# Performance work log

Measured on AMD Instinct MI355X. Metric: run time of the kernel, lower is better.

Reference implementation:

```python
import jax, jax.numpy as jnp
import numpy as np

MEMORY_LENGTH = 32   # past states remembered
N_TARGETS = 3        # leak sources
T_STEPS = 1000       # duration / dt
DT = 0.1
HIDDEN = 128         # policy MLP hidden width
N_AGENTS = 1024      # vmapped batch of rollouts
IN_DIM = MEMORY_LENGTH * 3 + MEMORY_LENGTH  # flattened x_hist + conc_hist


def setup_inputs() -> dict:
    key = jax.random.key(0)
    k0, k1, k2, k3, k4 = jax.random.split(key, 5)
    target_pos = jax.random.normal(k0, (N_TARGETS, 2), dtype=jnp.float32) * 5.0
    logsigma = jax.random.normal(k1, (N_TARGETS,), dtype=jnp.float32) * 0.5
    x_inits = jax.random.normal(k2, (N_AGENTS, 3), dtype=jnp.float32) * 2.0
    W1 = jax.random.normal(k3, (HIDDEN, IN_DIM), dtype=jnp.float32) / np.sqrt(IN_DIM).astype(np.float32)
    b1 = jnp.zeros((HIDDEN,), dtype=jnp.float32)
    W2 = jax.random.normal(k4, (2, HIDDEN), dtype=jnp.float32) / np.sqrt(HIDDEN).astype(np.float32)
    b2 = jnp.zeros((2,), dtype=jnp.float32)
    return {"target_pos": target_pos, "logsigma": logsigma, "x_inits": x_inits,
            "W1": W1, "b1": b1, "W2": W2, "b2": b2}


def _concentration(x, y, target_pos, sigma):
    # x, y: [N]; target_pos: [nt, 2]; sigma: [nt] -> conc: [N]
    d2 = (x[:, None] - target_pos[None, :, 0]) ** 2 + (y[:, None] - target_pos[None, :, 1]) ** 2
    return ((1.0 / sigma) * jnp.exp(-d2 / sigma)).sum(-1)


def reference(target_pos, logsigma, x_inits, W1, b1, W2, b2):
    sigma = jnp.exp(logsigma)
    N = x_inits.shape[0]
    # initial histories: memory_length copies of the initial state / concentration
    x_hist0 = jnp.tile(x_inits[:, None, :], (1, MEMORY_LENGTH, 1))        # [N, M, 3]
    conc0 = _concentration(x_inits[:, 0], x_inits[:, 1], target_pos, sigma)
    conc_hist0 = jnp.tile(conc0[:, None], (1, MEMORY_LENGTH))             # [N, M]

    def step(carry, _):
        x_hist, conc_hist, x_cur = carry
        # policy MLP on flattened histories -> tanh controls (v, omega)
        feats = jnp.concatenate([x_hist.reshape(N, -1), conc_hist], axis=-1)  # [N, 4M]
        h = jax.nn.relu(feats @ W1.T + b1)
        u = jnp.tanh(h @ W2.T + b2)                                            # [N, 2]
        v, w = u[:, 0], u[:, 1]
        th = x_cur[:, 2]
        # Dubins car dynamics (zero actuation noise)
        x_next = x_cur + DT * jnp.stack([v * jnp.cos(th), v * jnp.sin(th), w], axis=-1)
        # shift histories: drop oldest, insert newest at front
        x_hist = jnp.concatenate([x_next[:, None, :], x_hist[:, :-1, :]], axis=1)
        c = _concentration(x_next[:, 0], x_next[:, 1], target_pos, sigma)
        conc_hist = jnp.concatenate([c[:, None], conc_hist[:, :-1]], axis=1)
        return (x_hist, conc_hist, x_next), (x_next, u)

    _, (traj, ctrl) = jax.lax.scan(step, (x_hist0, conc_hist0, x_inits), None, length=T_STEPS)
    # traj: [T, N, 3], ctrl: [T, N, 2]
    d2 = ((traj[:, :, 0][..., None] - target_pos[None, None, :, 0]) ** 2
          + (traj[:, :, 1][..., None] - target_pos[None, None, :, 1]) ** 2)   # [T, N, nt]
    per_target = (-1.0 / sigma) * jnp.exp(-d2 / sigma)                        # [T, N, nt]
    cost = per_target.mean(axis=(0, 1)).sum() + (ctrl ** 2).mean()
    return cost
```

## Files before the change

### kernel.cpp

```cpp
#include <hip/hip_runtime.h>

#define T_STEPS 1000
#define DT 0.1f
#define HIDDEN 128
#define N_AGENTS 1024

typedef float v2f __attribute__((ext_vector_type(2)));

__device__ __forceinline__ float tanh_fast(float x) {
    float e = __expf(2.0f * x);
    return 1.0f - 2.0f * __builtin_amdgcn_rcpf(e + 1.0f);
}

__device__ __forceinline__ v2f opaque_load8(const float* p) {
    v2f v;
    asm volatile("global_load_dwordx2 %0, %1, off\n\ts_waitcnt vmcnt(0)"
                 : "=v"(v)
                 : "v"((unsigned long long)(uintptr_t)p)
                 : "memory");
    return v;
}

__device__ __forceinline__ float uniformf(float v) {
    return __builtin_bit_cast(float,
        __builtin_amdgcn_readfirstlane(__builtin_bit_cast(int, v)));
}

__device__ __forceinline__ float wave_sum_dpp(float x) {
    float t;
    #define DPPADD(ctrl, rmask)                                              \
        t = __builtin_bit_cast(float, __builtin_amdgcn_update_dpp(           \
                0, __builtin_bit_cast(int, x), ctrl, rmask, 0xf, false));    \
        x += t;
    DPPADD(0x111, 0xf)
    DPPADD(0x112, 0xf)
    DPPADD(0x114, 0xf)
    DPPADD(0x118, 0xf)
    DPPADD(0x142, 0xa)
    DPPADD(0x143, 0xc)
    #undef DPPADD
    return __builtin_bit_cast(float,
        __builtin_amdgcn_readlane(__builtin_bit_cast(int, x), 63));
}

__global__ void pack_kernel(const float* __restrict__ W1,
                            float* __restrict__ pw) {
    const int row = blockIdx.x;
    const int a   = threadIdx.x;
    const float* rp = W1 + row * 128;
    float* out = pw + row * 128;
    out[2*a]          = rp[3*a];
    out[2*a + 1]      = rp[3*a + 1];
    out[64 + 2*a]     = rp[3*a + 2];
    out[64 + 2*a + 1] = rp[96 + a];
}

__global__ __launch_bounds__(128)
__attribute__((amdgpu_waves_per_eu(2, 2)))
void sim_kernel(const float* __restrict__ target_pos,
                const float* __restrict__ logsigma,
                const float* __restrict__ x_inits,
                const float* __restrict__ pw,
                const float* __restrict__ b1,
                const float* __restrict__ W2,
                const float* __restrict__ b2,
                float2* __restrict__ ws) {
    const int agent = blockIdx.x;
    const int tid  = threadIdx.x;
    const int h    = tid >> 6;
    const int lane = tid & 63;
    const int rowA = lane;
    const int rowB = lane + 64;

    __shared__ float2 part1[32][64];
    __shared__ float4 e4buf[16];

    const float tx0 = uniformf(target_pos[0]), ty0 = uniformf(target_pos[1]);
    const float tx1 = uniformf(target_pos[2]), ty1 = uniformf(target_pos[3]);
    const float tx2 = uniformf(target_pos[4]), ty2 = uniformf(target_pos[5]);
    const float is0 = uniformf(1.0f / expf(logsigma[0]));
    const float is1 = uniformf(1.0f / expf(logsigma[1]));
    const float is2 = uniformf(1.0f / expf(logsigma[2]));

    v2f WxyA[16], WzcA[16], WxyB[16], WzcB[16];
    {
        const float* baseA = pw + rowA * 128;
        const float* baseB = pw + rowB * 128;
        #pragma unroll
        for (int i = 0; i < 16; ++i) {
            WxyA[i] = opaque_load8(baseA + 32 * h + 2 * i);
            WzcA[i] = opaque_load8(baseA + 64 + 32 * h + 2 * i);
            WxyB[i] = opaque_load8(baseB + 32 * h + 2 * i);
            WzcB[i] = opaque_load8(baseB + 64 + 32 * h + 2 * i);
        }
    }
    const float b1A = b1[rowA], b1B = b1[rowB];
    const float w20A = W2[rowA], w20B = W2[rowB];
    const float w21A = W2[HIDDEN + rowA], w21B = W2[HIDDEN + rowB];
    const float b2x = uniformf(b2[0]), b2y = uniformf(b2[1]);

    auto conc = [&](float px, float py) {
        float dx0 = px - tx0, dy0 = py - ty0;
        float dx1 = px - tx1, dy1 = py - ty1;
        float dx2 = px - tx2, dy2 = py - ty2;
        float cc  = is0 * __expf(-(dx0*dx0 + dy0*dy0) * is0);
        cc       += is1 * __expf(-(dx1*dx1 + dy1*dy1) * is1);
        cc       += is2 * __expf(-(dx2*dx2 + dy2*dy2) * is2);
        return cc;
    };

    float x  = uniformf(x_inits[3 * agent]);
    float y  = uniformf(x_inits[3 * agent + 1]);
    float th = uniformf(x_inits[3 * agent + 2]);
    float c  = conc(x, y);

    v2f RA[16], RB[16];
    {
        v2f exy0 = {x, y}, ezc0 = {th, c};
        if (h == 0) {
            v2f aA = {0.f,0.f}, aB = {0.f,0.f};
            #pragma unroll
            for (int k = 15; k >= 0; --k) {
                aA = WxyA[k]*exy0 + aA;  aA = WzcA[k]*ezc0 + aA;
                aB = WxyB[k]*exy0 + aB;  aB = WzcB[k]*ezc0 + aB;
                RA[k] = aA;  RB[k] = aB;
            }
            if (lane == 0) {
                float4 e0 = make_float4(x, y, th, c);
                #pragma unroll
                for (int m = 9; m < 16; ++m) e4buf[m] = e0;
                e4buf[0] = e0;
            }
        } else {
            RA[8] = (v2f){0.f,0.f};  RB[8] = (v2f){0.f,0.f};
            v2f aA = {0.f,0.f}, aB = {0.f,0.f};
            #pragma unroll
            for (int k = 15; k >= 1; --k) {
                aA = WxyA[k]*exy0 + aA;  aA = WzcA[k]*ezc0 + aA;
                aB = WxyB[k]*exy0 + aB;  aB = WzcB[k]*ezc0 + aB;
                RA[(k+8)&15] = aA;  RB[(k+8)&15] = aB;
            }
            v2f fA = WxyA[0]*exy0 + aA;  fA = WzcA[0]*ezc0 + fA;
            v2f fB = WxyB[0]*exy0 + aB;  fB = WzcB[0]*ezc0 + fB;
            float2 full = make_float2(fA.x + fA.y, fB.x + fB.y);
            #pragma unroll
            for (int s = 0; s <= 8; ++s) part1[s][lane] = full;
        }
    }
    __syncthreads();

    float S_c = 0.f, S_u = 0.f;

    if (h == 0) {
        float2 pl = part1[0][lane];
        auto h0_step = [&](int j, int s16) {
            float hA = fmaxf((RA[j].x + RA[j].y) + pl.x + b1A, 0.f);
            float hB = fmaxf((RB[j].x + RB[j].y) + pl.y + b1B, 0.f);
            float s0 = wave_sum_dpp(fmaf(w20A, hA, w20B * hB));
            float s1 = wave_sum_dpp(fmaf(w21A, hA, w21B * hB));
            float v  = tanh_fast(s0 + b2x);
            float wv = tanh_fast(s1 + b2y);
            S_u += v * v + wv * wv;
            float sn = __sinf(th), cs = __cosf(th);
            float dv = DT * v;
            x  = fmaf(dv, cs, x);
            y  = fmaf(dv, sn, y);
            th = fmaf(DT, wv, th);
            c  = conc(x, y);
            S_c += c;
            if (lane == 0) e4buf[(j + 1) & 15] = make_float4(x, y, th, c);
            v2f exy = {x, y}, ezc = {th, c};
            RA[j] = WxyA[15] * exy;  RA[j] = WzcA[15] * ezc + RA[j];
            RB[j] = WxyB[15] * exy;  RB[j] = WzcB[15] * ezc + RB[j];
            #pragma unroll
            for (int k = 0; k < 15; ++k) {
                const int m = (j + 1 + k) & 15;
                RA[m] = WxyA[k] * exy + RA[m];  RA[m] = WzcA[k] * ezc + RA[m];
                RB[m] = WxyB[k] * exy + RB[m];  RB[m] = WzcB[k] * ezc + RB[m];
            }
            pl = part1[(s16 + j + 1) & 31][lane];
        };
        #pragma unroll 1
        for (int tt = 0; tt < 62; ++tt) {
            const int s16 = (tt & 1) << 4;
            __syncthreads();
            #pragma unroll
            for (int j = 0; j < 8; ++j) h0_step(j, s16);
            __syncthreads();
            #pragma unroll
            for (int j = 8; j < 16; ++j) h0_step(j, s16);
        }
        __syncthreads();
        #pragma unroll
        for (int j = 0; j < 8; ++j) h0_step(j, 0);

        if (lane == 0) ws[agent] = make_float2(S_c, S_u);
    } else {
        auto h1_step = [&](int j, int s16) {
            float4 e = e4buf[(j + 9) & 15];
            v2f exy = {e.x, e.y}, ezc = {e.z, e.w};
            {
                const int m = (j + 8) & 15;
                RA[m] = WxyA[15] * exy;  RA[m] = WzcA[15] * ezc + RA[m];
                RB[m] = WxyB[15] * exy;  RB[m] = WzcB[15] * ezc + RB[m];
            }
            #pragma unroll
            for (int k = 0; k < 15; ++k) {
                const int m = (j + 9 + k) & 15;
                RA[m] = WxyA[k] * exy + RA[m];  RA[m] = WzcA[k] * ezc + RA[m];
                RB[m] = WxyB[k] * exy + RB[m];  RB[m] = WzcB[k] * ezc + RB[m];
            }
            {
                const int m = (j + 9) & 15;
                part1[(s16 + j + 9) & 31][lane] =
                    make_float2(RA[m].x + RA[m].y, RB[m].x + RB[m].y);
            }
        };
        #pragma unroll 1
        for (int tt = 0; tt < 62; ++tt) {
            const int s16 = (tt & 1) << 4;
            __syncthreads();
            #pragma unroll
            for (int j = 0; j < 8; ++j) h1_step(j, s16);
            __syncthreads();
            #pragma unroll
            for (int j = 8; j < 16; ++j) h1_step(j, s16);
        }
        __syncthreads();
        #pragma unroll
        for (int j = 0; j < 8; ++j) h1_step(j, 0);
    }
}

__global__ void reduce_kernel(const float2* __restrict__ ws,
                              float* __restrict__ out) {
    const int tid = threadIdx.x;
    float sc = 0.f, su = 0.f;
    for (int i = tid; i < N_AGENTS; i += 256) {
        float2 v = ws[i];
        sc += v.x;
        su += v.y;
    }
    #pragma unroll
    for (int off = 32; off > 0; off >>= 1) {
        sc += __shfl_xor(sc, off);
        su += __shfl_xor(su, off);
    }
    __shared__ float2 partw[4];
    int wave = tid >> 6;
    if ((tid & 63) == 0) partw[wave] = make_float2(sc, su);
    __syncthreads();
    if (tid == 0) {
        float SC = partw[0].x + partw[1].x + partw[2].x + partw[3].x;
        float SU = partw[0].y + partw[1].y + partw[2].y + partw[3].y;
        const float invNT  = 1.0f / (float)(N_AGENTS * T_STEPS);
        const float invNT2 = 1.0f / (float)(N_AGENTS * T_STEPS * 2);
        out[0] = -SC * invNT + SU * invNT2;
    }
}

extern "C" void kernel_launch(void* const* d_in, const int* in_sizes, int n_in,
                              void* d_out, int out_size, void* d_ws, size_t ws_size,
                              hipStream_t stream) {
    const float* target_pos = (const float*)d_in[0];
    const float* logsigma   = (const float*)d_in[1];
    const float* x_inits    = (const float*)d_in[2];
    const float* W1         = (const float*)d_in[3];
    const float* b1         = (const float*)d_in[4];
    const float* W2         = (const float*)d_in[5];
    const float* b2         = (const float*)d_in[6];

    float*  pw   = (float*)d_ws;
    float2* sums = (float2*)((char*)d_ws + 64 * 1024);

    pack_kernel<<<HIDDEN, 32, 0, stream>>>(W1, pw);
    sim_kernel<<<N_AGENTS, 128, 0, stream>>>(target_pos, logsigma, x_inits,
                                             pw, b1, W2, b2, sums);
    reduce_kernel<<<1, 256, 0, stream>>>(sums, (float*)d_out);
}
```

Baseline: 655.3 us.

## Batch history-weight accumulation four steps at a time off the serial critical path

The wave that runs the sequential step loop now applies only the few weight updates needed for the next steps immediately. It defers the rest of the 16-deep history accumulation into a batched update after every four steps, which shortens the per-step latency chain. The helper wave likewise processes four history entries per batch using a sliding 20-entry accumulator, then writes partial sums and shifts. This cuts per-step dependency latency and lets the FMAs interleave better, at the cost of higher register pressure and more intricate index bookkeeping.

```diff
diff --git a/kernel.cpp b/kernel.cpp
--- a/kernel.cpp
+++ b/kernel.cpp
@@ -114,10 +114,10 @@
     float th = uniformf(x_inits[3 * agent + 2]);
     float c  = conc(x, y);
 
-    v2f RA[16], RB[16];
-    {
-        v2f exy0 = {x, y}, ezc0 = {th, c};
-        if (h == 0) {
+    if (h == 0) {
+        v2f RA[16], RB[16];
+        {
+            v2f exy0 = {x, y}, ezc0 = {th, c};
             v2f aA = {0.f,0.f}, aB = {0.f,0.f};
             #pragma unroll
             for (int k = 15; k >= 0; --k) {
@@ -131,31 +131,17 @@
                 for (int m = 9; m < 16; ++m) e4buf[m] = e0;
                 e4buf[0] = e0;
             }
-        } else {
-            RA[8] = (v2f){0.f,0.f};  RB[8] = (v2f){0.f,0.f};
-            v2f aA = {0.f,0.f}, aB = {0.f,0.f};
-            #pragma unroll
-            for (int k = 15; k >= 1; --k) {
-                aA = WxyA[k]*exy0 + aA;  aA = WzcA[k]*ezc0 + aA;
-                aB = WxyB[k]*exy0 + aB;  aB = WzcB[k]*ezc0 + aB;
-                RA[(k+8)&15] = aA;  RB[(k+8)&15] = aB;
-            }
-            v2f fA = WxyA[0]*exy0 + aA;  fA = WzcA[0]*ezc0 + fA;
-            v2f fB = WxyB[0]*exy0 + aB;  fB = WzcB[0]*ezc0 + fB;
-            float2 full = make_float2(fA.x + fA.y, fB.x + fB.y);
-            #pragma unroll
-            for (int s = 0; s <= 8; ++s) part1[s][lane] = full;
-        }
-    }
-    __syncthreads();
-
-    float S_c = 0.f, S_u = 0.f;
-
-    if (h == 0) {
+        }
+        __syncthreads();
         float2 pl = part1[0][lane];
+        v2f es_xy[4], es_zc[4];
+        float S_c = 0.f, S_u = 0.f;
+
         auto h0_step = [&](int j, int s16) {
             float hA = fmaxf((RA[j].x + RA[j].y) + pl.x + b1A, 0.f);
             float hB = fmaxf((RB[j].x + RB[j].y) + pl.y + b1B, 0.f);
+            RA[j] = (v2f){0.f, 0.f};
+            RB[j] = (v2f){0.f, 0.f};
             float s0 = wave_sum_dpp(fmaf(w20A, hA, w20B * hB));
             float s1 = wave_sum_dpp(fmaf(w21A, hA, w21B * hB));
             float v  = tanh_fast(s0 + b2x);
@@ -170,65 +156,121 @@
             S_c += c;
             if (lane == 0) e4buf[(j + 1) & 15] = make_float4(x, y, th, c);
             v2f exy = {x, y}, ezc = {th, c};
-            RA[j] = WxyA[15] * exy;  RA[j] = WzcA[15] * ezc + RA[j];
-            RB[j] = WxyB[15] * exy;  RB[j] = WzcB[15] * ezc + RB[j];
-            #pragma unroll
-            for (int k = 0; k < 15; ++k) {
-                const int m = (j + 1 + k) & 15;
-                RA[m] = WxyA[k] * exy + RA[m];  RA[m] = WzcA[k] * ezc + RA[m];
-                RB[m] = WxyB[k] * exy + RB[m];  RB[m] = WzcB[k] * ezc + RB[m];
+            es_xy[j & 3] = exy;  es_zc[j & 3] = ezc;
+            #pragma unroll
+            for (int k = 0; k < 3; ++k) {
+                if (k <= 2 - (j & 3)) {
+                    const int m = (j + 1 + k) & 15;
+                    RA[m] = WxyA[k]*exy + RA[m];  RA[m] = WzcA[k]*ezc + RA[m];
+                    RB[m] = WxyB[k]*exy + RB[m];  RB[m] = WzcB[k]*ezc + RB[m];
+                }
             }
             pl = part1[(s16 + j + 1) & 31][lane];
         };
+        auto h0_batch = [&](int q) {
+            #pragma unroll
+            for (int kk = 0; kk < 16; ++kk) {
+                #pragma unroll
+                for (int i = 0; i < 4; ++i) {
+                    if (kk >= 3 - i) {
+                        const int m = (4*q + i + 1 + kk) & 15;
+                        RA[m] = WxyA[kk]*es_xy[i] + RA[m];
+                        RA[m] = WzcA[kk]*es_zc[i] + RA[m];
+                        RB[m] = WxyB[kk]*es_xy[i] + RB[m];
+                        RB[m] = WzcB[kk]*es_zc[i] + RB[m];
+                    }
+                }
+            }
+        };
+
         #pragma unroll 1
-        for (int tt = 0; tt < 62; ++tt) {
-            const int s16 = (tt & 1) << 4;
+        for (int b = 0; b < 62; ++b) {
+            const int s16 = (b & 1) << 4;
             __syncthreads();
             #pragma unroll
-            for (int j = 0; j < 8; ++j) h0_step(j, s16);
+            for (int j = 0; j < 4; ++j) h0_step(j, s16);
+            h0_batch(0);
+            #pragma unroll
+            for (int j = 4; j < 8; ++j) h0_step(j, s16);
+            h0_batch(1);
             __syncthreads();
             #pragma unroll
-            for (int j = 8; j < 16; ++j) h0_step(j, s16);
+            for (int j = 8; j < 12; ++j) h0_step(j, s16);
+            h0_batch(2);
+            #pragma unroll
+            for (int j = 12; j < 16; ++j) h0_step(j, s16);
+            h0_batch(3);
         }
         __syncthreads();
         #pragma unroll
-        for (int j = 0; j < 8; ++j) h0_step(j, 0);
+        for (int j = 0; j < 4; ++j) h0_step(j, 0);
+        h0_batch(0);
+        #pragma unroll
+        for (int j = 4; j < 8; ++j) h0_step(j, 0);
 
         if (lane == 0) ws[agent] = make_float2(S_c, S_u);
     } else {
-        auto h1_step = [&](int j, int s16) {
-            float4 e = e4buf[(j + 9) & 15];
-            v2f exy = {e.x, e.y}, ezc = {e.z, e.w};
-            {
-                const int m = (j + 8) & 15;
-                RA[m] = WxyA[15] * exy;  RA[m] = WzcA[15] * ezc + RA[m];
-                RB[m] = WxyB[15] * exy;  RB[m] = WzcB[15] * ezc + RB[m];
-            }
-            #pragma unroll
-            for (int k = 0; k < 15; ++k) {
-                const int m = (j + 9 + k) & 15;
-                RA[m] = WxyA[k] * exy + RA[m];  RA[m] = WzcA[k] * ezc + RA[m];
-                RB[m] = WxyB[k] * exy + RB[m];  RB[m] = WzcB[k] * ezc + RB[m];
-            }
-            {
-                const int m = (j + 9) & 15;
-                part1[(s16 + j + 9) & 31][lane] =
-                    make_float2(RA[m].x + RA[m].y, RB[m].x + RB[m].y);
-            }
+        v2f PA[20], PB[20];
+        {
+            v2f exy0 = {x, y}, ezc0 = {th, c};
+            #pragma unroll
+            for (int i = 15; i < 20; ++i) { PA[i] = (v2f){0.f,0.f}; PB[i] = (v2f){0.f,0.f}; }
+            v2f aA = {0.f,0.f}, aB = {0.f,0.f};
+            #pragma unroll
+            for (int k = 15; k >= 1; --k) {
+                aA = WxyA[k]*exy0 + aA;  aA = WzcA[k]*ezc0 + aA;
+                aB = WxyB[k]*exy0 + aB;  aB = WzcB[k]*ezc0 + aB;
+                PA[k-1] = aA;  PB[k-1] = aB;
+            }
+            v2f fA = WxyA[0]*exy0 + aA;  fA = WzcA[0]*ezc0 + fA;
+            v2f fB = WxyB[0]*exy0 + aB;  fB = WzcB[0]*ezc0 + fB;
+            float2 full = make_float2(fA.x + fA.y, fB.x + fB.y);
+            #pragma unroll
+            for (int s = 0; s <= 8; ++s) part1[s][lane] = full;
+        }
+        __syncthreads();
+
+        auto h1_batch = [&](int n, int b1w) {
+            v2f pxy[4], pzc[4];
+            #pragma unroll
+            for (int i = 0; i < 4; ++i) {
+                float4 e = e4buf[(9 + 4*n + i) & 15];
+                pxy[i] = (v2f){e.x, e.y};
+                pzc[i] = (v2f){e.z, e.w};
+            }
+            #pragma unroll
+            for (int kk = 0; kk < 16; ++kk) {
+                #pragma unroll
+                for (int i = 0; i < 4; ++i) {
+                    const int idx = i + kk;
+                    PA[idx] = WxyA[kk]*pxy[i] + PA[idx];
+                    PA[idx] = WzcA[kk]*pzc[i] + PA[idx];
+                    PB[idx] = WxyB[kk]*pxy[i] + PB[idx];
+                    PB[idx] = WzcB[kk]*pzc[i] + PB[idx];
+                }
+            }
+            #pragma unroll
+            for (int i = 0; i < 4; ++i) {
+                part1[(b1w * 16 + 9 + 4*n + i) & 31][lane] =
+                    make_float2(PA[i].x + PA[i].y, PB[i].x + PB[i].y);
+            }
+            #pragma unroll
+            for (int i = 0; i < 16; ++i) { PA[i] = PA[i+4]; PB[i] = PB[i+4]; }
+            #pragma unroll
+            for (int i = 16; i < 20; ++i) { PA[i] = (v2f){0.f,0.f}; PB[i] = (v2f){0.f,0.f}; }
         };
+
         #pragma unroll 1
-        for (int tt = 0; tt < 62; ++tt) {
-            const int s16 = (tt & 1) << 4;
+        for (int b = 0; b < 62; ++b) {
+            const int b1w = b & 1;
             __syncthreads();
-            #pragma unroll
-            for (int j = 0; j < 8; ++j) h1_step(j, s16);
+            h1_batch(0, b1w);
+            h1_batch(1, b1w);
             __syncthreads();
-            #pragma unroll
-            for (int j = 8; j < 16; ++j) h1_step(j, s16);
+            h1_batch(2, b1w);
+            h1_batch(3, b1w);
         }
         __syncthreads();
-        #pragma unroll
-        for (int j = 0; j < 8; ++j) h1_step(j, 0);
     }
 }
 
```

New measurement: 651.6 us. About the same (-0.6%).
